# Kernel optimization log

Hardware: AMD Instinct MI355X
Metric: run time of the kernel (lower is better)

## Reference

```python
import jax, jax.numpy as jnp
import numpy as np

B, L, E, D1, D2 = 256, 128, 64, 512, 512


def setup_inputs() -> dict:
    key = jax.random.key(0)
    k1, k2, k3, kw = jax.random.split(key, 4)
    tensor1 = jax.random.normal(k1, (B, L, D1), dtype=jnp.float32)
    tensor2 = jax.random.normal(k2, (B, L, D2), dtype=jnp.float32)
    parameters_index = jax.random.randint(k3, (B,), 0, E, dtype=jnp.int32)
    # xavier_uniform with relu gain: gain*sqrt(6/(fan_in+fan_out)),
    # torch fan for [E,D1,D2]: fan_in = D1*D2, fan_out = E*D2
    gain = float(np.sqrt(2.0))
    bound = gain * float(np.sqrt(6.0 / (D1 * D2 + E * D2)))
    weights = jax.random.uniform(kw, (E, D1, D2), minval=-bound, maxval=bound, dtype=jnp.float32)
    return {"tensor1": tensor1, "tensor2": tensor2, "parameters_index": parameters_index, "weights": weights}


def reference(tensor1, tensor2, parameters_index, weights):
    # gather per-batch weight matrix [B, D1, D2], then bilinear form x1^T W x2
    w = weights[parameters_index]  # [B, D1, D2]
    # equals: sum over i,j of tensor1[b,l,i] * w[b,i,j] * tensor2[b,l,j] -> [B, L]
    return jnp.einsum('bli,bij,blj->bl', tensor1, w, tensor2)
```

## Files before the change

kernel.cpp:

```cpp
#include <hip/hip_runtime.h>
#include <stdint.h>

#define NB 256
#define NL 128
#define ND1 512
#define ND2 512
#define NE 64

#define BI 256
#define BK 64
#define NKT (ND2 / BK)
#define LDST 72

typedef float float4_t __attribute__((ext_vector_type(4)));
typedef __bf16 bf16x8_t __attribute__((ext_vector_type(8)));
typedef unsigned short ushort4_t __attribute__((ext_vector_type(4)));
typedef unsigned short ushort8_t __attribute__((ext_vector_type(8)));

__device__ __forceinline__ unsigned short f2bf(float f) {
    unsigned int u = __float_as_uint(f);
    u += 0x7FFFu + ((u >> 16) & 1u);
    return (unsigned short)(u >> 16);
}

__device__ __forceinline__ ushort4_t cvt4(float4_t v) {
    ushort4_t u;
    u.x = f2bf(v.x); u.y = f2bf(v.y); u.z = f2bf(v.z); u.w = f2bf(v.w);
    return u;
}

__global__ void sort_kernel(const int* __restrict__ pidx, int* __restrict__ perm)
{
    __shared__ int cnt[NE];
    __shared__ int base[NE];
    const int t = threadIdx.x;
    if (t < NE) cnt[t] = 0;
    __syncthreads();
    const int e = pidx[t];
    const int r = atomicAdd(&cnt[e], 1);
    __syncthreads();
    if (t == 0) {
        int s = 0;
        for (int i = 0; i < NE; ++i) { base[i] = s; s += cnt[i]; }
    }
    __syncthreads();
    perm[base[e] + r] = t;
}

template <bool USE_PERM>
__global__ __launch_bounds__(512, 4) void pdot_kernel(
    const float* __restrict__ t1, const float* __restrict__ t2,
    const int* __restrict__ pidx, const float* __restrict__ wgt,
    const int* __restrict__ perm, float* __restrict__ out)
{
    __shared__ unsigned short sA[NL * LDST];
    __shared__ unsigned short sB[BI * LDST];

    const int g  = blockIdx.x;
    const int slot = (g & 7) * 32 + ((g >> 3) & 31);
    const int b  = USE_PERM ? perm[slot] : (g & (NB - 1));
    const int it = g >> 8;
    const int i0 = it * BI;

    const int t  = threadIdx.x;
    const int w  = t >> 6;
    const int wv = w & 3;
    const int ih = w >> 2;
    const int ln = t & 63;
    const int nh = ln & 15;
    const int qd = ln >> 4;

    const int e = pidx[b];
    const float* aPtr  = t2  + (size_t)b * (NL * ND2);
    const float* bPtr  = wgt + (size_t)e * (ND1 * ND2) + (size_t)i0 * ND2;
    const float* t1p   = t1  + (size_t)b * (NL * ND1) + i0 + ih * 128;

    float4_t acc[2][8];
    #pragma unroll
    for (int i = 0; i < 2; ++i)
        #pragma unroll
        for (int j = 0; j < 8; ++j) {
            float4_t z = {0.f, 0.f, 0.f, 0.f};
            acc[i][j] = z;
        }

    const int s_row = t >> 4;
    const int s_kq  = (t & 15) * 4;
    const size_t sOff = (size_t)s_row * ND2 + s_kq;

    float4_t pa[4], pb[8];

    #pragma unroll
    for (int p = 0; p < 4; ++p)
        pa[p] = *(const float4_t*)(aPtr + sOff + (size_t)p * (32 * ND2));
    #pragma unroll
    for (int p = 0; p < 8; ++p)
        pb[p] = *(const float4_t*)(bPtr + sOff + (size_t)p * (32 * ND2));
    #pragma unroll
    for (int p = 0; p < 4; ++p) {
        const int row = p * 32 + s_row;
        *(ushort4_t*)(&sA[row * LDST + s_kq]) = cvt4(pa[p]);
    }
    #pragma unroll
    for (int p = 0; p < 8; ++p) {
        const int row = p * 32 + s_row;
        *(ushort4_t*)(&sB[row * LDST + s_kq]) = cvt4(pb[p]);
    }
    #pragma unroll
    for (int p = 0; p < 4; ++p)
        pa[p] = *(const float4_t*)(aPtr + sOff + BK + (size_t)p * (32 * ND2));
    #pragma unroll
    for (int p = 0; p < 8; ++p)
        pb[p] = *(const float4_t*)(bPtr + sOff + BK + (size_t)p * (32 * ND2));
    __builtin_amdgcn_sched_barrier(0);
    asm volatile("s_waitcnt lgkmcnt(0)" ::: "memory");
    __builtin_amdgcn_sched_barrier(0);
    __builtin_amdgcn_s_barrier();
    __builtin_amdgcn_sched_barrier(0);

    for (int kt = 0; kt < NKT; ++kt) {
        #pragma unroll
        for (int ks = 0; ks < 2; ++ks) {
            const int kf = ks * 32 + qd * 8;
            const int ra = wv * 32 + nh;
            bf16x8_t af0 = __builtin_bit_cast(bf16x8_t, *(ushort8_t*)(&sA[(ra     ) * LDST + kf]));
            bf16x8_t af1 = __builtin_bit_cast(bf16x8_t, *(ushort8_t*)(&sA[(ra + 16) * LDST + kf]));
            #pragma unroll
            for (int ns = 0; ns < 8; ++ns) {
                bf16x8_t bv = __builtin_bit_cast(bf16x8_t, *(ushort8_t*)(&sB[(ih * 128 + ns * 16 + nh) * LDST + kf]));
                acc[0][ns] = __builtin_amdgcn_mfma_f32_16x16x32_bf16(af0, bv, acc[0][ns], 0, 0, 0);
                acc[1][ns] = __builtin_amdgcn_mfma_f32_16x16x32_bf16(af1, bv, acc[1][ns], 0, 0, 0);
            }
        }

        if (kt < NKT - 1) {
            __builtin_amdgcn_sched_barrier(0);
            __builtin_amdgcn_s_barrier();
            __builtin_amdgcn_sched_barrier(0);

            #pragma unroll
            for (int p = 0; p < 4; ++p) {
                const int row = p * 32 + s_row;
                *(ushort4_t*)(&sA[row * LDST + s_kq]) = cvt4(pa[p]);
            }
            #pragma unroll
            for (int p = 0; p < 8; ++p) {
                const int row = p * 32 + s_row;
                *(ushort4_t*)(&sB[row * LDST + s_kq]) = cvt4(pb[p]);
            }
            if (kt < NKT - 2) {
                const size_t k0 = (size_t)(kt + 2) * BK;
                #pragma unroll
                for (int p = 0; p < 4; ++p)
                    pa[p] = *(const float4_t*)(aPtr + sOff + k0 + (size_t)p * (32 * ND2));
                #pragma unroll
                for (int p = 0; p < 8; ++p)
                    pb[p] = *(const float4_t*)(bPtr + sOff + k0 + (size_t)p * (32 * ND2));
            }
            __builtin_amdgcn_sched_barrier(0);
            asm volatile("s_waitcnt lgkmcnt(0)" ::: "memory");
            __builtin_amdgcn_sched_barrier(0);
            __builtin_amdgcn_s_barrier();
            __builtin_amdgcn_sched_barrier(0);
        }
    }

    #pragma unroll
    for (int ms = 0; ms < 2; ++ms) {
        #pragma unroll
        for (int r = 0; r < 4; ++r) {
            const int row = wv * 32 + ms * 16 + qd * 4 + r;
            float ps = 0.f;
            #pragma unroll
            for (int ns = 0; ns < 8; ++ns) {
                const float tv = t1p[(size_t)row * ND1 + ns * 16 + nh];
                ps += acc[ms][ns][r] * tv;
            }
            ps += __shfl_xor(ps, 1);
            ps += __shfl_xor(ps, 2);
            ps += __shfl_xor(ps, 4);
            ps += __shfl_xor(ps, 8);
            if (nh == 0) atomicAdd(&out[b * NL + row], ps);
        }
    }
}

extern "C" void kernel_launch(void* const* d_in, const int* in_sizes, int n_in,
                              void* d_out, int out_size, void* d_ws, size_t ws_size,
                              hipStream_t stream)
{
    const float* t1  = (const float*)d_in[0];
    const float* t2  = (const float*)d_in[1];
    const int* pidx  = (const int*)d_in[2];
    const float* wgt = (const float*)d_in[3];
    float* out = (float*)d_out;

    hipMemsetAsync(out, 0, (size_t)out_size * sizeof(float), stream);

    if (ws_size >= NB * sizeof(int)) {
        int* perm = (int*)d_ws;
        sort_kernel<<<dim3(1), dim3(NB), 0, stream>>>(pidx, perm);
        pdot_kernel<true><<<dim3(NB * (ND1 / BI)), dim3(512), 0, stream>>>(t1, t2, pidx, wgt, perm, out);
    } else {
        pdot_kernel<false><<<dim3(NB * (ND1 / BI)), dim3(512), 0, stream>>>(t1, t2, pidx, wgt, nullptr, out);
    }
}
```

Baseline: 218.3 us.

## Halve I-tile, double-buffer LDS, interleave stores with MFMA, fuse memset into sort

Shrinks the per-block D1 tile from 256 to 128, doubling the grid to 1024 blocks, and halves the per-thread accumulators. Shared memory becomes double-buffered, so the next tile's bf16 stores are interleaved between the two MFMA halves, dropping one barrier per k-step. It also raises wave priority around the MFMAs and folds the output memset into the sort kernel, saving a launch. In exchange, each weight/t2 tile is loaded by twice as many blocks, increasing global traffic for t2.

```diff
diff --git a/kernel.cpp b/kernel.cpp
--- a/kernel.cpp
+++ b/kernel.cpp
@@ -7,10 +7,11 @@
 #define ND2 512
 #define NE 64
 
-#define BI 256
+#define BI 128
 #define BK 64
 #define NKT (ND2 / BK)
 #define LDST 72
+#define BUFSZ ((NL + BI) * LDST)
 
 typedef float float4_t __attribute__((ext_vector_type(4)));
 typedef __bf16 bf16x8_t __attribute__((ext_vector_type(8)));
@@ -29,22 +30,27 @@
     return u;
 }
 
-__global__ void sort_kernel(const int* __restrict__ pidx, int* __restrict__ perm)
+__global__ void pre_kernel(const int* __restrict__ pidx, int* __restrict__ perm,
+                           float* __restrict__ out, int zero_n, int do_sort)
 {
-    __shared__ int cnt[NE];
-    __shared__ int base[NE];
-    const int t = threadIdx.x;
-    if (t < NE) cnt[t] = 0;
-    __syncthreads();
-    const int e = pidx[t];
-    const int r = atomicAdd(&cnt[e], 1);
-    __syncthreads();
-    if (t == 0) {
-        int s = 0;
-        for (int i = 0; i < NE; ++i) { base[i] = s; s += cnt[i]; }
-    }
-    __syncthreads();
-    perm[base[e] + r] = t;
+    const int g = blockIdx.x, t = threadIdx.x;
+    const int idx = g * 256 + t;
+    if (idx < zero_n) out[idx] = 0.f;
+    if (do_sort && g == 0) {
+        __shared__ int cnt[NE];
+        __shared__ int base[NE];
+        if (t < NE) cnt[t] = 0;
+        __syncthreads();
+        const int e = pidx[t];
+        const int r = atomicAdd(&cnt[e], 1);
+        __syncthreads();
+        if (t == 0) {
+            int s = 0;
+            for (int i = 0; i < NE; ++i) { base[i] = s; s += cnt[i]; }
+        }
+        __syncthreads();
+        perm[base[e] + r] = t;
+    }
 }
 
 template <bool USE_PERM>
@@ -53,13 +59,14 @@
     const int* __restrict__ pidx, const float* __restrict__ wgt,
     const int* __restrict__ perm, float* __restrict__ out)
 {
-    __shared__ unsigned short sA[NL * LDST];
-    __shared__ unsigned short sB[BI * LDST];
+    __shared__ unsigned short sm[2][BUFSZ];
 
     const int g  = blockIdx.x;
-    const int slot = (g & 7) * 32 + ((g >> 3) & 31);
-    const int b  = USE_PERM ? perm[slot] : (g & (NB - 1));
-    const int it = g >> 8;
+    const int x  = g & 7;
+    const int s  = g >> 3;
+    const int slot = x * 32 + (s >> 2);
+    const int b  = USE_PERM ? perm[slot] : slot;
+    const int it = s & 3;
     const int i0 = it * BI;
 
     const int t  = threadIdx.x;
@@ -71,15 +78,15 @@
     const int qd = ln >> 4;
 
     const int e = pidx[b];
-    const float* aPtr  = t2  + (size_t)b * (NL * ND2);
-    const float* bPtr  = wgt + (size_t)e * (ND1 * ND2) + (size_t)i0 * ND2;
-    const float* t1p   = t1  + (size_t)b * (NL * ND1) + i0 + ih * 128;
-
-    float4_t acc[2][8];
+    const float* aPtr = t2  + (size_t)b * (NL * ND2);
+    const float* bPtr = wgt + (size_t)e * (ND1 * ND2) + (size_t)i0 * ND2;
+    const float* t1p  = t1  + (size_t)b * (NL * ND1) + i0 + ih * 64;
+
+    float4_t acc[2][4];
     #pragma unroll
     for (int i = 0; i < 2; ++i)
         #pragma unroll
-        for (int j = 0; j < 8; ++j) {
+        for (int j = 0; j < 4; ++j) {
             float4_t z = {0.f, 0.f, 0.f, 0.f};
             acc[i][j] = z;
         }
@@ -87,77 +94,94 @@
     const int s_row = t >> 4;
     const int s_kq  = (t & 15) * 4;
     const size_t sOff = (size_t)s_row * ND2 + s_kq;
-
-    float4_t pa[4], pb[8];
-
-    #pragma unroll
-    for (int p = 0; p < 4; ++p)
+    const int wOff  = s_row * LDST + s_kq;
+    const int wOffB = (NL + s_row) * LDST + s_kq;
+
+    float4_t pa[4], pb[4];
+
+    #pragma unroll
+    for (int p = 0; p < 4; ++p) {
         pa[p] = *(const float4_t*)(aPtr + sOff + (size_t)p * (32 * ND2));
-    #pragma unroll
-    for (int p = 0; p < 8; ++p)
         pb[p] = *(const float4_t*)(bPtr + sOff + (size_t)p * (32 * ND2));
+    }
     #pragma unroll
     for (int p = 0; p < 4; ++p) {
-        const int row = p * 32 + s_row;
-        *(ushort4_t*)(&sA[row * LDST + s_kq]) = cvt4(pa[p]);
-    }
-    #pragma unroll
-    for (int p = 0; p < 8; ++p) {
-        const int row = p * 32 + s_row;
-        *(ushort4_t*)(&sB[row * LDST + s_kq]) = cvt4(pb[p]);
-    }
-    #pragma unroll
-    for (int p = 0; p < 4; ++p)
+        *(ushort4_t*)(&sm[0][wOff  + p * (32 * LDST)]) = cvt4(pa[p]);
+        *(ushort4_t*)(&sm[0][wOffB + p * (32 * LDST)]) = cvt4(pb[p]);
+    }
+    #pragma unroll
+    for (int p = 0; p < 4; ++p) {
         pa[p] = *(const float4_t*)(aPtr + sOff + BK + (size_t)p * (32 * ND2));
-    #pragma unroll
-    for (int p = 0; p < 8; ++p)
         pb[p] = *(const float4_t*)(bPtr + sOff + BK + (size_t)p * (32 * ND2));
+    }
     __builtin_amdgcn_sched_barrier(0);
     asm volatile("s_waitcnt lgkmcnt(0)" ::: "memory");
     __builtin_amdgcn_sched_barrier(0);
     __builtin_amdgcn_s_barrier();
     __builtin_amdgcn_sched_barrier(0);
 
+    #pragma unroll
     for (int kt = 0; kt < NKT; ++kt) {
-        #pragma unroll
-        for (int ks = 0; ks < 2; ++ks) {
-            const int kf = ks * 32 + qd * 8;
+        const int cur = kt & 1;
+        const int nxt = cur ^ 1;
+        const unsigned short* cA = &sm[cur][0];
+        const unsigned short* cB = &sm[cur][NL * LDST];
+
+        {
+            const int kf = qd * 8;
             const int ra = wv * 32 + nh;
-            bf16x8_t af0 = __builtin_bit_cast(bf16x8_t, *(ushort8_t*)(&sA[(ra     ) * LDST + kf]));
-            bf16x8_t af1 = __builtin_bit_cast(bf16x8_t, *(ushort8_t*)(&sA[(ra + 16) * LDST + kf]));
-            #pragma unroll
-            for (int ns = 0; ns < 8; ++ns) {
-                bf16x8_t bv = __builtin_bit_cast(bf16x8_t, *(ushort8_t*)(&sB[(ih * 128 + ns * 16 + nh) * LDST + kf]));
-                acc[0][ns] = __builtin_amdgcn_mfma_f32_16x16x32_bf16(af0, bv, acc[0][ns], 0, 0, 0);
-                acc[1][ns] = __builtin_amdgcn_mfma_f32_16x16x32_bf16(af1, bv, acc[1][ns], 0, 0, 0);
-            }
+            bf16x8_t af0 = __builtin_bit_cast(bf16x8_t, *(const ushort8_t*)(&cA[(ra     ) * LDST + kf]));
+            bf16x8_t af1 = __builtin_bit_cast(bf16x8_t, *(const ushort8_t*)(&cA[(ra + 16) * LDST + kf]));
+            bf16x8_t bv[4];
+            #pragma unroll
+            for (int ns = 0; ns < 4; ++ns)
+                bv[ns] = __builtin_bit_cast(bf16x8_t, *(const ushort8_t*)(&cB[(ih * 64 + ns * 16 + nh) * LDST + kf]));
+            __builtin_amdgcn_s_setprio(1);
+            #pragma unroll
+            for (int ns = 0; ns < 4; ++ns) {
+                acc[0][ns] = __builtin_amdgcn_mfma_f32_16x16x32_bf16(af0, bv[ns], acc[0][ns], 0, 0, 0);
+                acc[1][ns] = __builtin_amdgcn_mfma_f32_16x16x32_bf16(af1, bv[ns], acc[1][ns], 0, 0, 0);
+            }
+            __builtin_amdgcn_s_setprio(0);
         }
 
         if (kt < NKT - 1) {
-            __builtin_amdgcn_sched_barrier(0);
-            __builtin_amdgcn_s_barrier();
-            __builtin_amdgcn_sched_barrier(0);
-
-            #pragma unroll
-            for (int p = 0; p < 4; ++p) {
-                const int row = p * 32 + s_row;
-                *(ushort4_t*)(&sA[row * LDST + s_kq]) = cvt4(pa[p]);
-            }
-            #pragma unroll
-            for (int p = 0; p < 8; ++p) {
-                const int row = p * 32 + s_row;
-                *(ushort4_t*)(&sB[row * LDST + s_kq]) = cvt4(pb[p]);
-            }
+            #pragma unroll
+            for (int p = 0; p < 4; ++p)
+                *(ushort4_t*)(&sm[nxt][wOff + p * (32 * LDST)]) = cvt4(pa[p]);
+        }
+
+        {
+            const int kf = 32 + qd * 8;
+            const int ra = wv * 32 + nh;
+            bf16x8_t af0 = __builtin_bit_cast(bf16x8_t, *(const ushort8_t*)(&cA[(ra     ) * LDST + kf]));
+            bf16x8_t af1 = __builtin_bit_cast(bf16x8_t, *(const ushort8_t*)(&cA[(ra + 16) * LDST + kf]));
+            bf16x8_t bv[4];
+            #pragma unroll
+            for (int ns = 0; ns < 4; ++ns)
+                bv[ns] = __builtin_bit_cast(bf16x8_t, *(const ushort8_t*)(&cB[(ih * 64 + ns * 16 + nh) * LDST + kf]));
+            __builtin_amdgcn_s_setprio(1);
+            #pragma unroll
+            for (int ns = 0; ns < 4; ++ns) {
+                acc[0][ns] = __builtin_amdgcn_mfma_f32_16x16x32_bf16(af0, bv[ns], acc[0][ns], 0, 0, 0);
+                acc[1][ns] = __builtin_amdgcn_mfma_f32_16x16x32_bf16(af1, bv[ns], acc[1][ns], 0, 0, 0);
+            }
+            __builtin_amdgcn_s_setprio(0);
+        }
+
+        if (kt < NKT - 1) {
+            #pragma unroll
+            for (int p = 0; p < 4; ++p)
+                *(ushort4_t*)(&sm[nxt][wOffB + p * (32 * LDST)]) = cvt4(pb[p]);
             if (kt < NKT - 2) {
                 const size_t k0 = (size_t)(kt + 2) * BK;
                 #pragma unroll
-                for (int p = 0; p < 4; ++p)
+                for (int p = 0; p < 4; ++p) {
                     pa[p] = *(const float4_t*)(aPtr + sOff + k0 + (size_t)p * (32 * ND2));
-                #pragma unroll
-                for (int p = 0; p < 8; ++p)
                     pb[p] = *(const float4_t*)(bPtr + sOff + k0 + (size_t)p * (32 * ND2));
-            }
-            __builtin_amdgcn_sched_barrier(0);
+                }
+                __builtin_amdgcn_sched_barrier(0);
+            }
             asm volatile("s_waitcnt lgkmcnt(0)" ::: "memory");
             __builtin_amdgcn_sched_barrier(0);
             __builtin_amdgcn_s_barrier();
@@ -172,7 +196,7 @@
             const int row = wv * 32 + ms * 16 + qd * 4 + r;
             float ps = 0.f;
             #pragma unroll
-            for (int ns = 0; ns < 8; ++ns) {
+            for (int ns = 0; ns < 4; ++ns) {
                 const float tv = t1p[(size_t)row * ND1 + ns * 16 + nh];
                 ps += acc[ms][ns][r] * tv;
             }
@@ -195,13 +219,14 @@
     const float* wgt = (const float*)d_in[3];
     float* out = (float*)d_out;
 
-    hipMemsetAsync(out, 0, (size_t)out_size * sizeof(float), stream);
-
-    if (ws_size >= NB * sizeof(int)) {
-        int* perm = (int*)d_ws;
-        sort_kernel<<<dim3(1), dim3(NB), 0, stream>>>(pidx, perm);
+    const int zero_blocks = (out_size + 255) / 256;
+    const bool have_ws = ws_size >= NB * sizeof(int);
+    int* perm = have_ws ? (int*)d_ws : nullptr;
+
+    pre_kernel<<<dim3(zero_blocks), dim3(256), 0, stream>>>(pidx, perm, out, out_size, have_ws ? 1 : 0);
+
+    if (have_ws)
         pdot_kernel<true><<<dim3(NB * (ND1 / BI)), dim3(512), 0, stream>>>(t1, t2, pidx, wgt, perm, out);
-    } else {
+    else
         pdot_kernel<false><<<dim3(NB * (ND1 / BI)), dim3(512), 0, stream>>>(t1, t2, pidx, wgt, nullptr, out);
-    }
-}
+}
```

Result: faster. 207.6 us (-4.9%).
